# Optimization experiments

Measured on AMD Instinct MI355X. Metric: run time of the kernel, lower is better.

Reference implementation:

```python
import jax, jax.numpy as jnp
import numpy as np

V, D, B, C = 50000, 256, 256, 10  # B must equal D (module's loss only broadcasts when B == embed_dim)


def setup_inputs() -> dict:
    key = jax.random.key(0)
    ks = jax.random.split(key, 14)
    s = 0.02
    return {
        "center_id": jax.random.randint(ks[0], (B,), 0, V),
        "context_ids": jax.random.randint(ks[1], (B, C), 0, V),
        "embeddings": jax.random.normal(ks[2], (V, D), jnp.float32) * s,
        "prior_means_w": jax.random.normal(ks[3], (V, D), jnp.float32) * s,
        "prior_vars_w": jax.random.normal(ks[4], (V, D), jnp.float32) * s,
        "enc_W": jax.random.normal(ks[5], (2 * D, 2 * D), jnp.float32) * s,
        "enc_b": jax.random.normal(ks[6], (2 * D,), jnp.float32) * s,
        "mean_W": jax.random.normal(ks[7], (D, 2 * D), jnp.float32) * s,
        "mean_b": jax.random.normal(ks[8], (D,), jnp.float32) * s,
        "var_W": jax.random.normal(ks[9], (D, 2 * D), jnp.float32) * s,
        "var_b": jax.random.normal(ks[10], (D,), jnp.float32) * s,
        "vocab_W": jax.random.normal(ks[11], (V, D), jnp.float32) * s,
        "vocab_b": jax.random.normal(ks[12], (V,), jnp.float32) * s,
        "epsilon": jax.random.normal(ks[13], (D,), jnp.float32),  # std_normal.sample(), shared across batch
    }


def reference(center_id, context_ids, embeddings, prior_means_w, prior_vars_w,
              enc_W, enc_b, mean_W, mean_b, var_W, var_b, vocab_W, vocab_b, epsilon):
    center = embeddings[center_id]            # [B, D]
    context = embeddings[context_ids]         # [B, C, D]
    enc_in = jnp.concatenate([jnp.broadcast_to(center[:, None, :], (B, C, D)), context], axis=2)  # [B, C, 2D]
    h = jax.nn.relu(jnp.einsum('bcd,ed->bce', enc_in, enc_W) + enc_b)
    h = jnp.sum(h, axis=1)                    # [B, 2D]
    mean = h @ mean_W.T + mean_b              # [B, D]
    var = jax.nn.softplus(h @ var_W.T + var_b)  # [B, D]
    z = mean + jnp.exp(var / 2.0) * epsilon   # reparameterization, one shared eps
    logits = z @ vocab_W.T + vocab_b          # [B, V]
    log_probs = jax.nn.log_softmax(logits, axis=1)
    # diagonal-Gaussian KL(q || prior), vectorized form of the per-row numpy kl_div
    prior_mean = prior_means_w[center_id]
    prior_var = jax.nn.softplus(prior_vars_w[center_id])
    kl = 0.5 * (jnp.sum(var / prior_var, axis=1)
                + jnp.sum((prior_mean - mean) ** 2 / prior_var, axis=1)
                - D
                + jnp.sum(jnp.log(prior_var) - jnp.log(var), axis=1))  # [B]
    # per-token NLL gather-sum (vectorized double Python loop)
    recon = jnp.sum(jnp.take_along_axis(log_probs, context_ids, axis=1), axis=1)  # [B]
    return jnp.sum(recon - kl)
```

## Files before the change

### kernel.cpp

```cpp
#include <hip/hip_runtime.h>
#include <hip/hip_bf16.h>

#define V 50000
#define D 256
#define B 256
#define C 10
#define TWO_D 512
#define VBLK 64
#define NBLK ((V + VBLK - 1) / VBLK)
#define MPAD 4096

typedef __bf16 bf16x8 __attribute__((ext_vector_type(8)));
typedef float f32x4 __attribute__((ext_vector_type(4)));
typedef unsigned short ushort_t;
typedef unsigned int uint_t;

__device__ inline ushort_t f2bf(float f) {
    uint_t u = __builtin_bit_cast(uint_t, f);
    uint_t r = (u + 0x7FFFu + ((u >> 16) & 1u)) >> 16;
    return (ushort_t)r;
}

__device__ inline float softplus_f(float x) {
    return (x > 0.f) ? (x + log1pf(__expf(-x))) : log1pf(__expf(x));
}

__device__ inline float wave_reduce(float v) {
    #pragma unroll
    for (int m = 1; m < 64; m <<= 1) v += __shfl_xor(v, m);
    return v;
}

__global__ __launch_bounds__(256) void k0_gather(
    const int* __restrict__ center_id, const int* __restrict__ context_ids,
    const float* __restrict__ embeddings, ushort_t* __restrict__ xbf)
{
    const int idx = blockIdx.x * 256 + threadIdx.x;
    const int m = idx >> 7;
    const int q = idx & 127;
    const int k = q * 4;
    const int b = m >> 4, c = m & 15;
    ushort4 o;
    if (k < D) {
        const float4 v = *(const float4*)(embeddings + center_id[b] * D + k);
        o.x = f2bf(v.x); o.y = f2bf(v.y); o.z = f2bf(v.z); o.w = f2bf(v.w);
    } else if (c < C) {
        const float4 v = *(const float4*)(embeddings + context_ids[b * C + c] * D + (k - D));
        o.x = f2bf(v.x); o.y = f2bf(v.y); o.z = f2bf(v.z); o.w = f2bf(v.w);
    } else {
        o.x = 0; o.y = 0; o.z = 0; o.w = 0;
    }
    *(ushort4*)(xbf + idx * 4) = o;
}

__global__ __launch_bounds__(256) void k_enc(
    const float* __restrict__ enc_W, const float* __restrict__ enc_b,
    const ushort_t* __restrict__ xbf, ushort_t* __restrict__ h_bf)
{
    __shared__ __align__(16) ushort_t wt[2][64 * 40];
    const int tid = threadIdx.x;
    const int mblk = blockIdx.x & 63;
    const int nblk = blockIdx.x >> 6;
    const int n0 = nblk * 64;
    const int wid = tid >> 6, lane = tid & 63;
    const int l15 = lane & 15, g = lane >> 4;

    const int r0 = tid >> 3, kq = tid & 7, r1 = r0 + 32;
    const float* src0 = enc_W + (n0 + r0) * TWO_D + kq * 4;
    const float* src1 = enc_W + (n0 + r1) * TWO_D + kq * 4;
    const int dst0 = r0 * 40 + kq * 4;
    const int dst1 = r1 * 40 + kq * 4;

    {
        const float4 na = *(const float4*)(src0);
        const float4 nb = *(const float4*)(src1);
        ushort4 pa, pb;
        pa.x = f2bf(na.x); pa.y = f2bf(na.y); pa.z = f2bf(na.z); pa.w = f2bf(na.w);
        pb.x = f2bf(nb.x); pb.y = f2bf(nb.y); pb.z = f2bf(nb.z); pb.w = f2bf(nb.w);
        *(ushort4*)(&wt[0][dst0]) = pa;
        *(ushort4*)(&wt[0][dst1]) = pb;
    }
    __syncthreads();

    const int rowA = mblk * 64 + wid * 16 + l15;
    f32x4 acc[4] = {};
    #pragma unroll 1
    for (int kk = 0; kk < 16; ++kk) {
        const int cur = kk & 1, nxt = cur ^ 1;
        float4 na, nb;
        if (kk < 15) {
            na = *(const float4*)(src0 + (kk + 1) * 32);
            nb = *(const float4*)(src1 + (kk + 1) * 32);
        }
        const bf16x8 A = *(const bf16x8*)(xbf + rowA * TWO_D + kk * 32 + g * 8);
        bf16x8 Bf[4];
        #pragma unroll
        for (int vt = 0; vt < 4; ++vt)
            Bf[vt] = *(const bf16x8*)(&wt[cur][(vt * 16 + l15) * 40 + g * 8]);
        #pragma unroll
        for (int vt = 0; vt < 4; ++vt)
            acc[vt] = __builtin_amdgcn_mfma_f32_16x16x32_bf16(A, Bf[vt], acc[vt], 0, 0, 0);
        if (kk < 15) {
            ushort4 pa, pb;
            pa.x = f2bf(na.x); pa.y = f2bf(na.y); pa.z = f2bf(na.z); pa.w = f2bf(na.w);
            pb.x = f2bf(nb.x); pb.y = f2bf(nb.y); pb.z = f2bf(nb.z); pb.w = f2bf(nb.w);
            *(ushort4*)(&wt[nxt][dst0]) = pa;
            *(ushort4*)(&wt[nxt][dst1]) = pb;
        }
        __syncthreads();
    }

    const int b = mblk * 4 + wid;
    #pragma unroll
    for (int vt = 0; vt < 4; ++vt) {
        const int j = n0 + vt * 16 + l15;
        const float bias = enc_b[j];
        float s = 0.f;
        #pragma unroll
        for (int r = 0; r < 4; ++r) {
            const int c = g * 4 + r;
            const float vv = acc[vt][r] + bias;
            s += (c < C) ? fmaxf(vv, 0.f) : 0.f;
        }
        s += __shfl_xor(s, 16);
        s += __shfl_xor(s, 32);
        if (g == 0) h_bf[b * TWO_D + j] = f2bf(s);
    }
}

__global__ __launch_bounds__(256) void k_heads(
    const float* __restrict__ mean_W, const float* __restrict__ mean_b,
    const float* __restrict__ var_W, const float* __restrict__ var_b,
    const ushort_t* __restrict__ h_bf, float* __restrict__ mv)
{
    __shared__ __align__(16) ushort_t wt[2][64 * 40];
    const int tid = threadIdx.x;
    const int mblk = blockIdx.x & 3;
    const int nblk = blockIdx.x >> 2;
    const int n0 = nblk * 64;
    const float* Wsrc = (nblk < 4) ? mean_W : var_W;
    const float* bsrc = (nblk < 4) ? mean_b : var_b;
    const int nloc = (nblk & 3) * 64;
    const int wid = tid >> 6, lane = tid & 63;
    const int l15 = lane & 15, g = lane >> 4;

    const int r0 = tid >> 3, kq = tid & 7, r1 = r0 + 32;
    const float* src0 = Wsrc + (nloc + r0) * TWO_D + kq * 4;
    const float* src1 = Wsrc + (nloc + r1) * TWO_D + kq * 4;
    const int dst0 = r0 * 40 + kq * 4;
    const int dst1 = r1 * 40 + kq * 4;

    {
        const float4 na = *(const float4*)(src0);
        const float4 nb = *(const float4*)(src1);
        ushort4 pa, pb;
        pa.x = f2bf(na.x); pa.y = f2bf(na.y); pa.z = f2bf(na.z); pa.w = f2bf(na.w);
        pb.x = f2bf(nb.x); pb.y = f2bf(nb.y); pb.z = f2bf(nb.z); pb.w = f2bf(nb.w);
        *(ushort4*)(&wt[0][dst0]) = pa;
        *(ushort4*)(&wt[0][dst1]) = pb;
    }
    __syncthreads();

    const int rowA = mblk * 64 + wid * 16 + l15;
    f32x4 acc[4] = {};
    #pragma unroll 1
    for (int kk = 0; kk < 16; ++kk) {
        const int cur = kk & 1, nxt = cur ^ 1;
        float4 na, nb;
        if (kk < 15) {
            na = *(const float4*)(src0 + (kk + 1) * 32);
            nb = *(const float4*)(src1 + (kk + 1) * 32);
        }
        const bf16x8 A = *(const bf16x8*)(h_bf + rowA * TWO_D + kk * 32 + g * 8);
        bf16x8 Bf[4];
        #pragma unroll
        for (int vt = 0; vt < 4; ++vt)
            Bf[vt] = *(const bf16x8*)(&wt[cur][(vt * 16 + l15) * 40 + g * 8]);
        #pragma unroll
        for (int vt = 0; vt < 4; ++vt)
            acc[vt] = __builtin_amdgcn_mfma_f32_16x16x32_bf16(A, Bf[vt], acc[vt], 0, 0, 0);
        if (kk < 15) {
            ushort4 pa, pb;
            pa.x = f2bf(na.x); pa.y = f2bf(na.y); pa.z = f2bf(na.z); pa.w = f2bf(na.w);
            pb.x = f2bf(nb.x); pb.y = f2bf(nb.y); pb.z = f2bf(nb.z); pb.w = f2bf(nb.w);
            *(ushort4*)(&wt[nxt][dst0]) = pa;
            *(ushort4*)(&wt[nxt][dst1]) = pb;
        }
        __syncthreads();
    }

    const int rowBase = mblk * 64 + wid * 16;
    #pragma unroll
    for (int vt = 0; vt < 4; ++vt) {
        const int col = n0 + vt * 16 + l15;
        const float bias = bsrc[nloc + vt * 16 + l15];
        #pragma unroll
        for (int r = 0; r < 4; ++r) {
            const int row = rowBase + g * 4 + r;
            mv[row * TWO_D + col] = acc[vt][r] + bias;
        }
    }
}

__global__ __launch_bounds__(256) void k_z(
    const int* __restrict__ center_id, const int* __restrict__ context_ids,
    const float* __restrict__ prior_means_w, const float* __restrict__ prior_vars_w,
    const float* __restrict__ vocab_W, const float* __restrict__ vocab_b,
    const float* __restrict__ epsilon, const float* __restrict__ mv,
    ushort_t* __restrict__ zp, float* __restrict__ base)
{
    __shared__ float red[8];
    __shared__ int cids[C];
    const int b = blockIdx.x, tid = threadIdx.x;
    const int cid = center_id[b];
    if (tid < C) cids[tid] = context_ids[b * C + tid];
    __syncthreads();

    const int i = tid;
    const float mean = mv[b * TWO_D + i];
    const float a    = mv[b * TWO_D + D + i];
    const float var  = softplus_f(a);
    const float z    = mean + __expf(0.5f * var) * epsilon[i];

    {
        const int mt  = b >> 4;
        const int kkz = i >> 5;
        const int lz  = ((i >> 3) & 3) * 16 + (b & 15);
        zp[(mt * 8 + kkz) * 512 + lz * 8 + (i & 7)] = f2bf(z);
    }

    const float pm = prior_means_w[cid * D + i];
    const float pv = softplus_f(prior_vars_w[cid * D + i]);
    const float dm = pm - mean;
    float klt = var / pv + dm * dm / pv - 1.f + __logf(pv) - __logf(var);

    float wsum = 0.f;
    #pragma unroll
    for (int c = 0; c < C; ++c) wsum += vocab_W[cids[c] * D + i];
    float p = z * wsum;

    klt = wave_reduce(klt);
    p = wave_reduce(p);
    const int wid = tid >> 6, lane = tid & 63;
    if (lane == 0) { red[wid] = klt; red[4 + wid] = p; }
    __syncthreads();
    if (tid == 0) {
        const float kl = 0.5f * (red[0] + red[1] + red[2] + red[3]);
        float cs = red[4] + red[5] + red[6] + red[7];
        #pragma unroll
        for (int c = 0; c < C; ++c) cs += vocab_b[cids[c]];
        base[b] = cs - kl;
    }
}

__global__ __launch_bounds__(256, 3) void k3_fused(
    const float* __restrict__ vocab_W, const float* __restrict__ vocab_b,
    const ushort_t* __restrict__ zp, float* __restrict__ psum)
{
    __shared__ __align__(16) ushort_t lds[64 * 256];

    const int tid = threadIdx.x;
    const int blk = blockIdx.x;
    const int v0 = blk * VBLK;
    const int wid = tid >> 6, lane = tid & 63;
    const int l15 = lane & 15, g = lane >> 4;

    float bias[4];
    bool vld[4];
    #pragma unroll
    for (int vt = 0; vt < 4; ++vt) {
        const int v = v0 + vt * 16 + l15;
        vld[vt] = (v < V);
        bias[vt] = vocab_b[min(v, V - 1)];
    }

    f32x4 st[16];
    const int maxidx = V * D - 4;
    #pragma unroll
    for (int j = 0; j < 16; ++j) {
        const int idx = min(v0 * D + j * 1024 + tid * 4, maxidx);
        const float* p = vocab_W + idx;
        asm volatile("global_load_dwordx4 %0, %1, off"
                     : "=v"(st[j]) : "v"(p) : "memory");
    }
    asm volatile("s_waitcnt vmcnt(0)" ::: "memory");
    __builtin_amdgcn_sched_barrier(0);

    #pragma unroll
    for (int j = 0; j < 16; ++j) {
        const int row = j * 4 + wid;
        ushort4 p;
        p.x = f2bf(st[j][0]); p.y = f2bf(st[j][1]);
        p.z = f2bf(st[j][2]); p.w = f2bf(st[j][3]);
        *(ushort4*)(lds + row * 256 + ((lane * 4) ^ ((row & 7) << 3))) = p;
    }
    __syncthreads();

    f32x4 acc[4][4] = {};
    #pragma unroll 2
    for (int kk = 0; kk < 8; ++kk) {
        bf16x8 A[4], Bf[4];
        #pragma unroll
        for (int bt = 0; bt < 4; ++bt) {
            const int mt = wid * 4 + bt;
            A[bt] = *(const bf16x8*)(zp + ((mt * 8 + kk) << 9) + (lane << 3));
        }
        #pragma unroll
        for (int vt = 0; vt < 4; ++vt) {
            const int row = vt * 16 + l15;
            Bf[vt] = *(const bf16x8*)(
                lds + row * 256 + ((kk * 32 + g * 8) ^ ((row & 7) << 3)));
        }
        #pragma unroll
        for (int bt = 0; bt < 4; ++bt)
            #pragma unroll
            for (int vt = 0; vt < 4; ++vt)
                acc[bt][vt] = __builtin_amdgcn_mfma_f32_16x16x32_bf16(
                    A[bt], Bf[vt], acc[bt][vt], 0, 0, 0);
    }

    #pragma unroll
    for (int bt = 0; bt < 4; ++bt) {
        #pragma unroll
        for (int r = 0; r < 4; ++r) {
            float s = 0.f;
            #pragma unroll
            for (int vt = 0; vt < 4; ++vt)
                s += vld[vt] ? __expf(acc[bt][vt][r] + bias[vt]) : 0.f;
            #pragma unroll
            for (int m = 1; m < 16; m <<= 1) s += __shfl_xor(s, m);
            if (l15 == 0) {
                const int brow = wid * 64 + bt * 16 + g * 4 + r;
                psum[blk * 256 + brow] = s;
            }
        }
    }
}

__global__ __launch_bounds__(256) void k4_lse(
    const float* __restrict__ psum, const float* __restrict__ base,
    float* __restrict__ outb)
{
    __shared__ float red[4];
    const int b = blockIdx.x, tid = threadIdx.x;
    float s = 0.f;
    for (int i = tid; i < NBLK; i += 256) s += psum[i * 256 + b];
    s = wave_reduce(s);
    if ((tid & 63) == 0) red[tid >> 6] = s;
    __syncthreads();
    if (tid == 0) {
        const float tot = red[0] + red[1] + red[2] + red[3];
        outb[b] = base[b] - (float)C * __logf(tot);
    }
}

__global__ __launch_bounds__(256) void k5_final(
    const float* __restrict__ outb, float* __restrict__ out)
{
    __shared__ float red[4];
    const int tid = threadIdx.x;
    float s = outb[tid];
    s = wave_reduce(s);
    if ((tid & 63) == 0) red[tid >> 6] = s;
    __syncthreads();
    if (tid == 0) out[0] = red[0] + red[1] + red[2] + red[3];
}

extern "C" void kernel_launch(void* const* d_in, const int* in_sizes, int n_in,
                              void* d_out, int out_size, void* d_ws, size_t ws_size,
                              hipStream_t stream)
{
    const int*   center_id     = (const int*)d_in[0];
    const int*   context_ids   = (const int*)d_in[1];
    const float* embeddings    = (const float*)d_in[2];
    const float* prior_means_w = (const float*)d_in[3];
    const float* prior_vars_w  = (const float*)d_in[4];
    const float* enc_W         = (const float*)d_in[5];
    const float* enc_b         = (const float*)d_in[6];
    const float* mean_W        = (const float*)d_in[7];
    const float* mean_b        = (const float*)d_in[8];
    const float* var_W         = (const float*)d_in[9];
    const float* var_b         = (const float*)d_in[10];
    const float* vocab_W       = (const float*)d_in[11];
    const float* vocab_b       = (const float*)d_in[12];
    const float* epsilon       = (const float*)d_in[13];

    char* ws = (char*)d_ws;
    ushort_t* xbf     = (ushort_t*)ws;  ws += (size_t)MPAD * TWO_D * 2;
    ushort_t* h_bf    = (ushort_t*)ws;  ws += (size_t)B * TWO_D * 2;
    float*    mv      = (float*)ws;     ws += (size_t)B * TWO_D * 4;
    ushort_t* zp      = (ushort_t*)ws;  ws += (size_t)B * D * 2;
    float*    base    = (float*)ws;     ws += B * 4;
    float*    outb    = (float*)ws;     ws += B * 4;
    float*    psum    = (float*)ws;

    hipLaunchKernelGGL(k0_gather, dim3(2048), dim3(256), 0, stream,
                       center_id, context_ids, embeddings, xbf);
    hipLaunchKernelGGL(k_enc, dim3(512), dim3(256), 0, stream,
                       enc_W, enc_b, xbf, h_bf);
    hipLaunchKernelGGL(k_heads, dim3(32), dim3(256), 0, stream,
                       mean_W, mean_b, var_W, var_b, h_bf, mv);
    hipLaunchKernelGGL(k_z, dim3(B), dim3(256), 0, stream,
                       center_id, context_ids, prior_means_w, prior_vars_w,
                       vocab_W, vocab_b, epsilon, mv, zp, base);
    hipLaunchKernelGGL(k3_fused, dim3(NBLK), dim3(256), 0, stream,
                       vocab_W, vocab_b, zp, psum);
    hipLaunchKernelGGL(k4_lse, dim3(B), dim3(256), 0, stream, psum, base, outb);
    hipLaunchKernelGGL(k5_final, dim3(1), dim3(256), 0, stream, outb, (float*)d_out);
}
```

Baseline: 62.02 us.

## Preload whole enc_W tile into swizzled LDS and drop per-step barriers

The encoder GEMM kernel now loads its entire 64x512 weight slab with 32 inline-asm dwordx4 loads up front, converts it to bf16 into a swizzled 64 KB LDS buffer in two waves, and then runs the k-loop without any per-iteration __syncthreads or double buffering. It also unrolls the k-loop by two and adds a launch-bounds occupancy hint. The goal is to replace a serialized load-convert-sync pipeline with one bulk memory burst. The cost is more registers for 32 float4 staging values and 64 KB of LDS per block, which limits how many blocks fit on a CU.

```diff
diff --git a/kernel.cpp b/kernel.cpp
--- a/kernel.cpp
+++ b/kernel.cpp
@@ -30,6 +30,11 @@
     for (int m = 1; m < 64; m <<= 1) v += __shfl_xor(v, m);
     return v;
 }
+
+#define SWAIT(N) do { \
+    asm volatile("s_waitcnt vmcnt(" #N ")" ::: "memory"); \
+    __builtin_amdgcn_sched_barrier(0); \
+} while (0)
 
 __global__ __launch_bounds__(256) void k0_gather(
     const int* __restrict__ center_id, const int* __restrict__ context_ids,
@@ -53,11 +58,12 @@
     *(ushort4*)(xbf + idx * 4) = o;
 }
 
-__global__ __launch_bounds__(256) void k_enc(
+__global__ __launch_bounds__(256, 2) void k_enc(
     const float* __restrict__ enc_W, const float* __restrict__ enc_b,
     const ushort_t* __restrict__ xbf, ushort_t* __restrict__ h_bf)
 {
-    __shared__ __align__(16) ushort_t wt[2][64 * 40];
+    __shared__ __align__(16) ushort_t lds[64 * 512];
+
     const int tid = threadIdx.x;
     const int mblk = blockIdx.x & 63;
     const int nblk = blockIdx.x >> 6;
@@ -65,49 +71,57 @@
     const int wid = tid >> 6, lane = tid & 63;
     const int l15 = lane & 15, g = lane >> 4;
 
-    const int r0 = tid >> 3, kq = tid & 7, r1 = r0 + 32;
-    const float* src0 = enc_W + (n0 + r0) * TWO_D + kq * 4;
-    const float* src1 = enc_W + (n0 + r1) * TWO_D + kq * 4;
-    const int dst0 = r0 * 40 + kq * 4;
-    const int dst1 = r1 * 40 + kq * 4;
-
-    {
-        const float4 na = *(const float4*)(src0);
-        const float4 nb = *(const float4*)(src1);
-        ushort4 pa, pb;
-        pa.x = f2bf(na.x); pa.y = f2bf(na.y); pa.z = f2bf(na.z); pa.w = f2bf(na.w);
-        pb.x = f2bf(nb.x); pb.y = f2bf(nb.y); pb.z = f2bf(nb.z); pb.w = f2bf(nb.w);
-        *(ushort4*)(&wt[0][dst0]) = pa;
-        *(ushort4*)(&wt[0][dst1]) = pb;
+    f32x4 s0[16], s1[16];
+    const float* tbase = enc_W + (size_t)n0 * TWO_D;
+    #pragma unroll
+    for (int j = 0; j < 16; ++j) {
+        const float* p = tbase + j * 1024 + tid * 4;
+        asm volatile("global_load_dwordx4 %0, %1, off"
+                     : "=v"(s0[j]) : "v"(p) : "memory");
+    }
+    #pragma unroll
+    for (int j = 0; j < 16; ++j) {
+        const float* p = tbase + 16384 + j * 1024 + tid * 4;
+        asm volatile("global_load_dwordx4 %0, %1, off"
+                     : "=v"(s1[j]) : "v"(p) : "memory");
+    }
+    SWAIT(16);
+    #pragma unroll
+    for (int j = 0; j < 16; ++j) {
+        const int row = j * 2 + (wid >> 1);
+        const int colu = (wid & 1) * 256 + lane * 4;
+        ushort4 p;
+        p.x = f2bf(s0[j][0]); p.y = f2bf(s0[j][1]);
+        p.z = f2bf(s0[j][2]); p.w = f2bf(s0[j][3]);
+        *(ushort4*)(lds + row * 512 + (colu ^ ((row & 7) << 3))) = p;
+    }
+    SWAIT(0);
+    #pragma unroll
+    for (int j = 0; j < 16; ++j) {
+        const int row = 32 + j * 2 + (wid >> 1);
+        const int colu = (wid & 1) * 256 + lane * 4;
+        ushort4 p;
+        p.x = f2bf(s1[j][0]); p.y = f2bf(s1[j][1]);
+        p.z = f2bf(s1[j][2]); p.w = f2bf(s1[j][3]);
+        *(ushort4*)(lds + row * 512 + (colu ^ ((row & 7) << 3))) = p;
     }
     __syncthreads();
 
     const int rowA = mblk * 64 + wid * 16 + l15;
     f32x4 acc[4] = {};
-    #pragma unroll 1
+    #pragma unroll 2
     for (int kk = 0; kk < 16; ++kk) {
-        const int cur = kk & 1, nxt = cur ^ 1;
-        float4 na, nb;
-        if (kk < 15) {
-            na = *(const float4*)(src0 + (kk + 1) * 32);
-            nb = *(const float4*)(src1 + (kk + 1) * 32);
-        }
-        const bf16x8 A = *(const bf16x8*)(xbf + rowA * TWO_D + kk * 32 + g * 8);
+        const bf16x8 A = *(const bf16x8*)(xbf + (size_t)rowA * TWO_D + kk * 32 + g * 8);
         bf16x8 Bf[4];
         #pragma unroll
-        for (int vt = 0; vt < 4; ++vt)
-            Bf[vt] = *(const bf16x8*)(&wt[cur][(vt * 16 + l15) * 40 + g * 8]);
+        for (int vt = 0; vt < 4; ++vt) {
+            const int row = vt * 16 + l15;
+            Bf[vt] = *(const bf16x8*)(
+                lds + row * 512 + ((kk * 32 + g * 8) ^ ((row & 7) << 3)));
+        }
         #pragma unroll
         for (int vt = 0; vt < 4; ++vt)
             acc[vt] = __builtin_amdgcn_mfma_f32_16x16x32_bf16(A, Bf[vt], acc[vt], 0, 0, 0);
-        if (kk < 15) {
-            ushort4 pa, pb;
-            pa.x = f2bf(na.x); pa.y = f2bf(na.y); pa.z = f2bf(na.z); pa.w = f2bf(na.w);
-            pb.x = f2bf(nb.x); pb.y = f2bf(nb.y); pb.z = f2bf(nb.z); pb.w = f2bf(nb.w);
-            *(ushort4*)(&wt[nxt][dst0]) = pa;
-            *(ushort4*)(&wt[nxt][dst1]) = pb;
-        }
-        __syncthreads();
     }
 
     const int b = mblk * 4 + wid;
@@ -283,8 +297,7 @@
         asm volatile("global_load_dwordx4 %0, %1, off"
                      : "=v"(st[j]) : "v"(p) : "memory");
     }
-    asm volatile("s_waitcnt vmcnt(0)" ::: "memory");
-    __builtin_amdgcn_sched_barrier(0);
+    SWAIT(0);
 
     #pragma unroll
     for (int j = 0; j < 16; ++j) {
```

Measured after the change: 58.52 us. 1.06x faster.
